# Optimization experiments

Hardware: AMD Instinct MI355X
Metric: run time of the kernel (lower is better)

The kernel has to match this reference:

```python
import jax, jax.numpy as jnp
import numpy as np

B, N, EM = 16, 1024, 768
D_K, D_V, H = 768, 768, 12

def setup_inputs() -> dict:
    key = jax.random.key(0)
    ks = jax.random.split(key, 4)
    s = 0.02
    x = jax.random.normal(ks[0], (B, N, EM), dtype=jnp.float32)
    W_qk = jax.random.normal(ks[1], (EM, 2 * D_K), dtype=jnp.float32) * s
    b_qk = jnp.zeros((2 * D_K,), dtype=jnp.float32)
    W_v = jax.random.normal(ks[2], (EM, D_V), dtype=jnp.float32) * s
    b_v = jnp.zeros((D_V,), dtype=jnp.float32)
    W_proj = jax.random.normal(ks[3], (D_V, EM), dtype=jnp.float32) * s
    b_proj = jnp.zeros((EM,), dtype=jnp.float32)
    return {"x": x, "W_qk": W_qk, "b_qk": b_qk, "W_v": W_v, "b_v": b_v,
            "W_proj": W_proj, "b_proj": b_proj}

def reference(x, W_qk, b_qk, W_v, b_v, W_proj, b_proj):
    b, n, _ = x.shape
    d = D_K // H  # per-head dim
    # qk Linear -> [B,N,2*d_K]; rearrange 'b n (h d qk) -> qk b h n d'
    # i.e. last dim splits as (h, d, 2) with qk fastest-varying.
    qk = (x @ W_qk + b_qk).reshape(b, n, H, d, 2)
    Q = jnp.transpose(qk[..., 0], (0, 2, 1, 3))  # [B,H,N,d]
    K = jnp.transpose(qk[..., 1], (0, 2, 1, 3))  # [B,H,N,d]
    V = (x @ W_v + b_v).reshape(b, n, H, D_V // H).transpose(0, 2, 1, 3)  # [B,H,N,dv]
    scores = jnp.einsum('bhqd,bhkd->bhqk', Q, K) / jnp.sqrt(jnp.float32(d))
    att = jax.nn.softmax(scores, axis=-1)  # dropout p=0 -> identity
    out = jnp.einsum('bhqk,bhkv->bhqv', att, V)  # [B,H,N,dv]
    out = out.transpose(0, 2, 1, 3).reshape(b, n, D_V)
    return out @ W_proj + b_proj
```

## Files before the change

kernel.cpp:

```cpp
#include <hip/hip_runtime.h>
#include <hip/hip_bf16.h>
#include <stdint.h>

typedef unsigned short u16;
typedef __bf16 bf16_t;
typedef bf16_t bf16x8 __attribute__((ext_vector_type(8)));
typedef short s16x4 __attribute__((ext_vector_type(4)));
typedef float f32x4 __attribute__((ext_vector_type(4)));

__device__ __forceinline__ u16 f2bf(float f) {
    union { float f; uint32_t i; } v; v.f = f;
    uint32_t i = v.i;
    uint32_t r = (i + 0x7FFFu + ((i >> 16) & 1u)) >> 16;
    return (u16)r;
}

__device__ __forceinline__ void gload_lds16(const u16* g, u16* l) {
    auto gp = (const __attribute__((address_space(1))) void*)g;
    auto lp = (__attribute__((address_space(3))) void*)(uintptr_t)l;
    __builtin_amdgcn_global_load_lds(gp, lp, 16, 0, 0);
}

__global__ void convert_f32_bf16_kernel(const float* __restrict__ src,
                                        u16* __restrict__ dst, int n4) {
    int i = blockIdx.x * blockDim.x + threadIdx.x;
    if (i < n4) {
        float4 v = ((const float4*)src)[i];
        ushort4 o;
        o.x = f2bf(v.x); o.y = f2bf(v.y); o.z = f2bf(v.z); o.w = f2bf(v.w);
        ((ushort4*)dst)[i] = o;
    }
}

__global__ void transpose_qk_kernel(const float* __restrict__ W, const float* __restrict__ b,
                                    u16* __restrict__ Wt, float* __restrict__ bp) {
    int k = blockIdx.x;
    const float* row = W + (size_t)k * 1536;
    for (int c = threadIdx.x; c < 1536; c += 256) {
        int qk = c & 1;
        int r  = qk * 768 + (c >> 7) * 64 + ((c >> 1) & 63);
        float s = qk ? 1.0f : 0.125f;
        Wt[(size_t)r * 768 + k] = f2bf(s * row[c]);
    }
    if (k == 0) {
        for (int c = threadIdx.x; c < 1536; c += 256) {
            int qk = c & 1;
            int r  = qk * 768 + (c >> 7) * 64 + ((c >> 1) & 63);
            bp[r] = (qk ? 1.0f : 0.125f) * b[c];
        }
    }
}

__global__ void transpose_sq2_kernel(const float* __restrict__ Wv, u16* __restrict__ Wvt,
                                     const float* __restrict__ Wp, u16* __restrict__ Wpt) {
    int id = blockIdx.x;
    const float* W = (id < 768) ? Wv : Wp;
    u16* Wt        = (id < 768) ? Wvt : Wpt;
    int k = (id < 768) ? id : (id - 768);
    const float* row = W + (size_t)k * 768;
    for (int n = threadIdx.x; n < 768; n += 256)
        Wt[(size_t)n * 768 + k] = f2bf(row[n]);
}

__global__ __launch_bounds__(256)
void gemm_qkv_kernel(const u16* __restrict__ A,
                     const u16* __restrict__ Wqkt, const u16* __restrict__ Wvt,
                     const float* __restrict__ bqkp, const float* __restrict__ bv,
                     u16* __restrict__ Qp, u16* __restrict__ Kp, u16* __restrict__ Vp) {
    __shared__ __attribute__((aligned(16))) u16 As[128 * 64];
    __shared__ __attribute__((aligned(16))) u16 Bs[128 * 64];
    const int K = 768;

    const int tid  = threadIdx.x;
    const int lane = tid & 63;
    const int wave = tid >> 6;
    const int l16  = lane & 15;
    const int quad = lane >> 4;
    const int cpx  = 2304 >> 3;
    const int swz  = ((int)blockIdx.x & 7) * cpx + ((int)blockIdx.x >> 3);
    const int mt   = swz / 18;
    const int nt   = swz % 18;
    const bool vmode = nt >= 12;
    const int m0 = mt * 128;
    const int n0 = (vmode ? nt - 12 : nt) * 128;
    const u16* Bt = vmode ? Wvt : Wqkt;
    const float* bias = vmode ? bv : bqkp;
    const int wm = (wave & 1) * 64;
    const int wn = (wave >> 1) * 64;

    f32x4 acc[4][4];
#pragma unroll
    for (int i = 0; i < 4; i++)
#pragma unroll
        for (int j = 0; j < 4; j++) acc[i][j] = (f32x4){0.f, 0.f, 0.f, 0.f};

    const int rs   = lane >> 3;
    const int gseg = (lane & 7) ^ rs;
    const u16* Ag[4]; const u16* Bg[4];
#pragma unroll
    for (int c = 0; c < 4; c++) {
        Ag[c] = A  + (size_t)(m0 + c * 32 + wave * 8 + rs) * K + gseg * 8;
        Bg[c] = Bt + (size_t)(n0 + c * 32 + wave * 8 + rs) * K + gseg * 8;
    }
    u16* AsW = As + wave * 512;
    u16* BsW = Bs + wave * 512;
    const int sw7 = l16 & 7;

    for (int k0 = 0; k0 < K; k0 += 64) {
#pragma unroll
        for (int c = 0; c < 4; c++) {
            gload_lds16(Ag[c] + k0, AsW + c * 2048);
            gload_lds16(Bg[c] + k0, BsW + c * 2048);
        }
        __syncthreads();

        bf16x8 af[4][2], bfr[4][2];
#pragma unroll
        for (int i = 0; i < 4; i++) {
#pragma unroll
            for (int hh = 0; hh < 2; hh++) {
                af[i][hh]  = *(const bf16x8*)&As[(wm + i * 16 + l16) * 64 +
                                                 (((hh * 4 + quad) ^ sw7) * 8)];
                bfr[i][hh] = *(const bf16x8*)&Bs[(wn + i * 16 + l16) * 64 +
                                                 (((hh * 4 + quad) ^ sw7) * 8)];
            }
        }
        if (vmode) {
#pragma unroll
            for (int i = 0; i < 4; i++)
#pragma unroll
                for (int j = 0; j < 4; j++)
#pragma unroll
                    for (int hh = 0; hh < 2; hh++)
                        acc[i][j] = __builtin_amdgcn_mfma_f32_16x16x32_bf16(af[i][hh], bfr[j][hh], acc[i][j], 0, 0, 0);
        } else {
#pragma unroll
            for (int i = 0; i < 4; i++)
#pragma unroll
                for (int j = 0; j < 4; j++)
#pragma unroll
                    for (int hh = 0; hh < 2; hh++)
                        acc[i][j] = __builtin_amdgcn_mfma_f32_16x16x32_bf16(bfr[j][hh], af[i][hh], acc[i][j], 0, 0, 0);
        }
        __syncthreads();
    }

    if (vmode) {
#pragma unroll
        for (int j = 0; j < 4; j++) {
            int cnb = n0 + wn + j * 16;
            int h   = cnb >> 6;
            int dv  = (cnb & 63) + l16;
            float bvv = bias[cnb + l16];
#pragma unroll
            for (int i = 0; i < 4; i++) {
                int cm = m0 + wm + i * 16 + quad * 4;
                int bb = cm >> 10, n = cm & 1023;
                ushort4 o;
                o.x = f2bf(acc[i][j][0] + bvv);
                o.y = f2bf(acc[i][j][1] + bvv);
                o.z = f2bf(acc[i][j][2] + bvv);
                o.w = f2bf(acc[i][j][3] + bvv);
                *(ushort4*)&Vp[((size_t)((bb * 12 + h) * 64 + dv)) * 1024 + n] = o;
            }
        }
    } else {
#pragma unroll
        for (int j = 0; j < 4; j++) {
            int f0 = n0 + wn + j * 16 + quad * 4;
            float4 bv4 = *(const float4*)&bias[f0];
            int qk = f0 >= 768;
            int hd = f0 - qk * 768;
            int h  = hd >> 6;
            int d0 = hd & 63;
            u16* dst = qk ? Kp : Qp;
#pragma unroll
            for (int i = 0; i < 4; i++) {
                int t = m0 + wm + i * 16 + l16;
                int bb = t >> 10, n = t & 1023;
                ushort4 o;
                o.x = f2bf(acc[i][j][0] + bv4.x);
                o.y = f2bf(acc[i][j][1] + bv4.y);
                o.z = f2bf(acc[i][j][2] + bv4.z);
                o.w = f2bf(acc[i][j][3] + bv4.w);
                *(ushort4*)&dst[((size_t)((bb * 12 + h) * 1024 + n)) * 64 + d0] = o;
            }
        }
    }
}

__global__ __launch_bounds__(256)
void gemm_out_kernel(const u16* __restrict__ A, const u16* __restrict__ Bt,
                     const float* __restrict__ bias, float* __restrict__ Cout,
                     int M, int N, int K) {
    __shared__ __attribute__((aligned(16))) u16 As[128 * 64];
    __shared__ __attribute__((aligned(16))) u16 Bs[128 * 64];

    const int tid  = threadIdx.x;
    const int lane = tid & 63;
    const int wave = tid >> 6;
    const int l16  = lane & 15;
    const int quad = lane >> 4;
    const int nxt = N >> 7;
    const int cpx = (int)gridDim.x >> 3;
    const int swz = ((int)blockIdx.x & 7) * cpx + ((int)blockIdx.x >> 3);
    const int m0 = (swz / nxt) * 128;
    const int n0 = (swz % nxt) * 128;
    const int wm = (wave & 1) * 64;
    const int wn = (wave >> 1) * 64;

    f32x4 acc[4][4];
#pragma unroll
    for (int i = 0; i < 4; i++)
#pragma unroll
        for (int j = 0; j < 4; j++) acc[i][j] = (f32x4){0.f, 0.f, 0.f, 0.f};

    const int rs   = lane >> 3;
    const int gseg = (lane & 7) ^ rs;
    const u16* Ag[4]; const u16* Bg[4];
#pragma unroll
    for (int c = 0; c < 4; c++) {
        Ag[c] = A  + (size_t)(m0 + c * 32 + wave * 8 + rs) * K + gseg * 8;
        Bg[c] = Bt + (size_t)(n0 + c * 32 + wave * 8 + rs) * K + gseg * 8;
    }
    u16* AsW = As + wave * 512;
    u16* BsW = Bs + wave * 512;
    const int sw7 = l16 & 7;

    for (int k0 = 0; k0 < K; k0 += 64) {
#pragma unroll
        for (int c = 0; c < 4; c++) {
            gload_lds16(Ag[c] + k0, AsW + c * 2048);
            gload_lds16(Bg[c] + k0, BsW + c * 2048);
        }
        __syncthreads();

        bf16x8 af[4][2], bfr[4][2];
#pragma unroll
        for (int i = 0; i < 4; i++) {
#pragma unroll
            for (int hh = 0; hh < 2; hh++) {
                af[i][hh]  = *(const bf16x8*)&As[(wm + i * 16 + l16) * 64 +
                                                 (((hh * 4 + quad) ^ sw7) * 8)];
                bfr[i][hh] = *(const bf16x8*)&Bs[(wn + i * 16 + l16) * 64 +
                                                 (((hh * 4 + quad) ^ sw7) * 8)];
            }
        }
#pragma unroll
        for (int i = 0; i < 4; i++)
#pragma unroll
            for (int j = 0; j < 4; j++)
#pragma unroll
                for (int hh = 0; hh < 2; hh++)
                    acc[i][j] = __builtin_amdgcn_mfma_f32_16x16x32_bf16(bfr[j][hh], af[i][hh], acc[i][j], 0, 0, 0);
        __syncthreads();
    }

#pragma unroll
    for (int j = 0; j < 4; j++) {
        int f0 = n0 + wn + j * 16 + quad * 4;
        float4 bv = *(const float4*)&bias[f0];
#pragma unroll
        for (int i = 0; i < 4; i++) {
            int t = m0 + wm + i * 16 + l16;
            float4 o;
            o.x = acc[i][j][0] + bv.x;
            o.y = acc[i][j][1] + bv.y;
            o.z = acc[i][j][2] + bv.z;
            o.w = acc[i][j][3] + bv.w;
            *(float4*)&Cout[(size_t)t * N + f0] = o;
        }
    }
}

__global__ __launch_bounds__(512)
void attention_mfma_kernel(const u16* __restrict__ Qp, const u16* __restrict__ Kp,
                           const u16* __restrict__ Vp, u16* __restrict__ attout) {
    __shared__ __attribute__((aligned(16))) u16 Ks[2][64 * 64];
    __shared__ __attribute__((aligned(16))) u16 Vs[2][64 * 64];

    const int tid  = threadIdx.x;
    const int wave = tid >> 6;
    const int lane = tid & 63;
    const int l16  = lane & 15;
    const int quad = lane >> 4;
    const int flat = blockIdx.x;
    const int swz  = (flat & 7) * 96 + (flat >> 3);
    const int bh   = swz >> 2;
    const int b    = bh / 12, h = bh % 12;
    const int q0   = (swz & 3) * 256 + wave * 32;

    const u16* Qhead = Qp + (size_t)bh * 1024 * 64;
    const u16* Khead = Kp + (size_t)bh * 1024 * 64;
    const u16* Vhead = Vp + (size_t)bh * 64 * 1024;

    bf16x8 qf[2][2];
#pragma unroll
    for (int qb = 0; qb < 2; qb++) {
        const u16* qrow = Qhead + (size_t)(q0 + qb * 16 + l16) * 64;
        qf[qb][0] = *(const bf16x8*)(qrow + quad * 8);
        qf[qb][1] = *(const bf16x8*)(qrow + 32 + quad * 8);
    }

    f32x4 oacc[2][4];
#pragma unroll
    for (int qb = 0; qb < 2; qb++)
#pragma unroll
        for (int db = 0; db < 4; db++) oacc[qb][db] = (f32x4){0.f, 0.f, 0.f, 0.f};
    float l_part[2] = {0.f, 0.f};

    const int srow = tid >> 3;
    const int gseg = (tid & 7) ^ (srow & 7);
    const u16* Kg = Khead + (size_t)srow * 64 + gseg * 8;
    const u16* Vg = Vhead + (size_t)srow * 1024 + gseg * 8;
    const int sw7 = l16 & 7;

    gload_lds16(Kg, &Ks[0][wave * 512]);
    gload_lds16(Vg, &Vs[0][wave * 512]);

    int cur = 0;
    for (int t = 0; t < 16; ++t) {
        __syncthreads();
        if (t < 15) {
            gload_lds16(Kg + (t + 1) * 4096, &Ks[cur ^ 1][wave * 512]);
            gload_lds16(Vg + (t + 1) * 64,   &Vs[cur ^ 1][wave * 512]);
        }
        const u16* Ksc = Ks[cur];
        const u16* Vsc = Vs[cur];

        union { uint32_t u[4]; bf16x8 v; } pf8[2][2];
        {
            bf16x8 kf[4][2];
#pragma unroll
            for (int jb = 0; jb < 4; jb++) {
#pragma unroll
                for (int hf = 0; hf < 2; hf++)
                    kf[jb][hf] = *(const bf16x8*)&Ksc[(jb * 16 + l16) * 64 +
                                                      (((hf * 4 + quad) ^ sw7) * 8)];
            }
#pragma unroll
            for (int qb = 0; qb < 2; qb++) {
#pragma unroll
                for (int jb = 0; jb < 4; jb++) {
                    f32x4 st = (f32x4){0.f, 0.f, 0.f, 0.f};
                    __builtin_amdgcn_s_setprio(1);
                    st = __builtin_amdgcn_mfma_f32_16x16x32_bf16(kf[jb][0], qf[qb][0], st, 0, 0, 0);
                    st = __builtin_amdgcn_mfma_f32_16x16x32_bf16(kf[jb][1], qf[qb][1], st, 0, 0, 0);
                    __builtin_amdgcn_s_setprio(0);
                    float e0 = __expf(st[0]), e1 = __expf(st[1]);
                    float e2 = __expf(st[2]), e3 = __expf(st[3]);
                    l_part[qb] += (e0 + e1) + (e2 + e3);
                    union { __hip_bfloat162 h2; uint32_t u; } c0, c1;
                    c0.h2 = __float22bfloat162_rn(make_float2(e0, e1));
                    c1.h2 = __float22bfloat162_rn(make_float2(e2, e3));
                    pf8[qb][jb >> 1].u[(jb & 1) * 2 + 0] = c0.u;
                    pf8[qb][jb >> 1].u[(jb & 1) * 2 + 1] = c1.u;
                }
            }
        }

        __builtin_amdgcn_s_setprio(1);
#pragma unroll
        for (int db = 0; db < 4; db++) {
#pragma unroll
            for (int jp = 0; jp < 2; jp++) {
                union { s16x4 hh[2]; bf16x8 v; } vb8;
                int glo = 4 * jp + (quad >> 1);
                int ghi = glo + 2;
                vb8.hh[0] = *(const s16x4*)&Vsc[(db * 16 + l16) * 64 +
                                                ((glo ^ sw7) * 8) + (quad & 1) * 4];
                vb8.hh[1] = *(const s16x4*)&Vsc[(db * 16 + l16) * 64 +
                                                ((ghi ^ sw7) * 8) + (quad & 1) * 4];
#pragma unroll
                for (int qb = 0; qb < 2; qb++)
                    oacc[qb][db] = __builtin_amdgcn_mfma_f32_16x16x32_bf16(
                        pf8[qb][jp].v, vb8.v, oacc[qb][db], 0, 0, 0);
            }
        }
        __builtin_amdgcn_s_setprio(0);
        cur ^= 1;
    }

#pragma unroll
    for (int qb = 0; qb < 2; qb++) {
        float l = l_part[qb];
        l += __shfl_xor(l, 16);
        l += __shfl_xor(l, 32);
        float linv[4];
#pragma unroll
        for (int r = 0; r < 4; r++)
            linv[r] = 1.0f / __shfl(l, quad * 4 + r);
        u16* orow = attout + (size_t)(b * 1024 + q0 + qb * 16 + quad * 4) * 768 + h * 64 + l16;
#pragma unroll
        for (int db = 0; db < 4; db++)
#pragma unroll
            for (int r = 0; r < 4; r++)
                orow[(size_t)r * 768 + db * 16] = f2bf(oacc[qb][db][r] * linv[r]);
    }
}

extern "C" void kernel_launch(void* const* d_in, const int* in_sizes, int n_in,
                              void* d_out, int out_size, void* d_ws, size_t ws_size,
                              hipStream_t stream) {
    const float* x      = (const float*)d_in[0];
    const float* W_qk   = (const float*)d_in[1];
    const float* b_qk   = (const float*)d_in[2];
    const float* W_v    = (const float*)d_in[3];
    const float* b_v    = (const float*)d_in[4];
    const float* W_proj = (const float*)d_in[5];
    const float* b_proj = (const float*)d_in[6];
    float* out = (float*)d_out;

    char* ws = (char*)d_ws;
    size_t off = 0;
    auto alloc = [&](size_t bytes) { void* p = ws + off; off += (bytes + 255) & ~255ull; return p; };
    u16*   xb     = (u16*)alloc((size_t)16384 * 768 * 2);
    u16*   Wqkt   = (u16*)alloc((size_t)1536 * 768 * 2);
    float* bqkp   = (float*)alloc(1536 * 4);
    u16*   Wvt    = (u16*)alloc((size_t)768 * 768 * 2);
    u16*   Wprojt = (u16*)alloc((size_t)768 * 768 * 2);
    u16*   Qp     = (u16*)alloc((size_t)16384 * 768 * 2);
    u16*   Kp     = (u16*)alloc((size_t)16384 * 768 * 2);
    u16*   Vp     = (u16*)alloc((size_t)16384 * 768 * 2);
    u16*   attout = (u16*)alloc((size_t)16384 * 768 * 2);

    convert_f32_bf16_kernel<<<12288, 256, 0, stream>>>(x, xb, 3145728);
    transpose_qk_kernel<<<768, 256, 0, stream>>>(W_qk, b_qk, Wqkt, bqkp);
    transpose_sq2_kernel<<<1536, 256, 0, stream>>>(W_v, Wvt, W_proj, Wprojt);

    gemm_qkv_kernel<<<2304, 256, 0, stream>>>(xb, Wqkt, Wvt, bqkp, b_v, Qp, Kp, Vp);
    attention_mfma_kernel<<<768, 512, 0, stream>>>(Qp, Kp, Vp, attout);
    gemm_out_kernel<<<768, 256, 0, stream>>>(attout, Wprojt, b_proj, out, 16384, 768, 768);
}
```

Baseline: 338.3 us.

## Double-buffer LDS tiles in QKV and output GEMMs to overlap loads with MFMA

Both projection GEMMs now use two LDS buffers per operand. The next k-tile is issued with global_load_lds while the current tile is consumed by MFMAs, and one of the two barriers per iteration is removed. Wave priority is raised around the MFMA block. This aims to hide global load latency, at the cost of doubling shared memory per block, which may lower occupancy.

Result: faster. 326.9 us (-3.4%).

```diff
diff --git a/kernel.cpp b/kernel.cpp
--- a/kernel.cpp
+++ b/kernel.cpp
@@ -67,8 +67,8 @@
                      const u16* __restrict__ Wqkt, const u16* __restrict__ Wvt,
                      const float* __restrict__ bqkp, const float* __restrict__ bv,
                      u16* __restrict__ Qp, u16* __restrict__ Kp, u16* __restrict__ Vp) {
-    __shared__ __attribute__((aligned(16))) u16 As[128 * 64];
-    __shared__ __attribute__((aligned(16))) u16 Bs[128 * 64];
+    __shared__ __attribute__((aligned(16))) u16 As[2][128 * 64];
+    __shared__ __attribute__((aligned(16))) u16 Bs[2][128 * 64];
     const int K = 768;
 
     const int tid  = threadIdx.x;
@@ -102,29 +102,39 @@
         Ag[c] = A  + (size_t)(m0 + c * 32 + wave * 8 + rs) * K + gseg * 8;
         Bg[c] = Bt + (size_t)(n0 + c * 32 + wave * 8 + rs) * K + gseg * 8;
     }
-    u16* AsW = As + wave * 512;
-    u16* BsW = Bs + wave * 512;
     const int sw7 = l16 & 7;
 
-    for (int k0 = 0; k0 < K; k0 += 64) {
-#pragma unroll
-        for (int c = 0; c < 4; c++) {
-            gload_lds16(Ag[c] + k0, AsW + c * 2048);
-            gload_lds16(Bg[c] + k0, BsW + c * 2048);
-        }
+#pragma unroll
+    for (int c = 0; c < 4; c++) {
+        gload_lds16(Ag[c], &As[0][wave * 512 + c * 2048]);
+        gload_lds16(Bg[c], &Bs[0][wave * 512 + c * 2048]);
+    }
+
+    int cur = 0;
+    for (int t = 0; t < 12; ++t) {
         __syncthreads();
+        if (t < 11) {
+#pragma unroll
+            for (int c = 0; c < 4; c++) {
+                gload_lds16(Ag[c] + (t + 1) * 64, &As[cur ^ 1][wave * 512 + c * 2048]);
+                gload_lds16(Bg[c] + (t + 1) * 64, &Bs[cur ^ 1][wave * 512 + c * 2048]);
+            }
+        }
+        const u16* Asc = As[cur];
+        const u16* Bsc = Bs[cur];
 
         bf16x8 af[4][2], bfr[4][2];
 #pragma unroll
         for (int i = 0; i < 4; i++) {
 #pragma unroll
             for (int hh = 0; hh < 2; hh++) {
-                af[i][hh]  = *(const bf16x8*)&As[(wm + i * 16 + l16) * 64 +
-                                                 (((hh * 4 + quad) ^ sw7) * 8)];
-                bfr[i][hh] = *(const bf16x8*)&Bs[(wn + i * 16 + l16) * 64 +
-                                                 (((hh * 4 + quad) ^ sw7) * 8)];
-            }
-        }
+                af[i][hh]  = *(const bf16x8*)&Asc[(wm + i * 16 + l16) * 64 +
+                                                  (((hh * 4 + quad) ^ sw7) * 8)];
+                bfr[i][hh] = *(const bf16x8*)&Bsc[(wn + i * 16 + l16) * 64 +
+                                                  (((hh * 4 + quad) ^ sw7) * 8)];
+            }
+        }
+        __builtin_amdgcn_s_setprio(1);
         if (vmode) {
 #pragma unroll
             for (int i = 0; i < 4; i++)
@@ -142,7 +152,8 @@
                     for (int hh = 0; hh < 2; hh++)
                         acc[i][j] = __builtin_amdgcn_mfma_f32_16x16x32_bf16(bfr[j][hh], af[i][hh], acc[i][j], 0, 0, 0);
         }
-        __syncthreads();
+        __builtin_amdgcn_s_setprio(0);
+        cur ^= 1;
     }
 
     if (vmode) {
@@ -193,8 +204,8 @@
 void gemm_out_kernel(const u16* __restrict__ A, const u16* __restrict__ Bt,
                      const float* __restrict__ bias, float* __restrict__ Cout,
                      int M, int N, int K) {
-    __shared__ __attribute__((aligned(16))) u16 As[128 * 64];
-    __shared__ __attribute__((aligned(16))) u16 Bs[128 * 64];
+    __shared__ __attribute__((aligned(16))) u16 As[2][128 * 64];
+    __shared__ __attribute__((aligned(16))) u16 Bs[2][128 * 64];
 
     const int tid  = threadIdx.x;
     const int lane = tid & 63;
@@ -223,29 +234,40 @@
         Ag[c] = A  + (size_t)(m0 + c * 32 + wave * 8 + rs) * K + gseg * 8;
         Bg[c] = Bt + (size_t)(n0 + c * 32 + wave * 8 + rs) * K + gseg * 8;
     }
-    u16* AsW = As + wave * 512;
-    u16* BsW = Bs + wave * 512;
     const int sw7 = l16 & 7;
-
-    for (int k0 = 0; k0 < K; k0 += 64) {
-#pragma unroll
-        for (int c = 0; c < 4; c++) {
-            gload_lds16(Ag[c] + k0, AsW + c * 2048);
-            gload_lds16(Bg[c] + k0, BsW + c * 2048);
-        }
+    const int nk = K >> 6;
+
+#pragma unroll
+    for (int c = 0; c < 4; c++) {
+        gload_lds16(Ag[c], &As[0][wave * 512 + c * 2048]);
+        gload_lds16(Bg[c], &Bs[0][wave * 512 + c * 2048]);
+    }
+
+    int cur = 0;
+    for (int t = 0; t < nk; ++t) {
         __syncthreads();
+        if (t < nk - 1) {
+#pragma unroll
+            for (int c = 0; c < 4; c++) {
+                gload_lds16(Ag[c] + (t + 1) * 64, &As[cur ^ 1][wave * 512 + c * 2048]);
+                gload_lds16(Bg[c] + (t + 1) * 64, &Bs[cur ^ 1][wave * 512 + c * 2048]);
+            }
+        }
+        const u16* Asc = As[cur];
+        const u16* Bsc = Bs[cur];
 
         bf16x8 af[4][2], bfr[4][2];
 #pragma unroll
         for (int i = 0; i < 4; i++) {
 #pragma unroll
             for (int hh = 0; hh < 2; hh++) {
-                af[i][hh]  = *(const bf16x8*)&As[(wm + i * 16 + l16) * 64 +
-                                                 (((hh * 4 + quad) ^ sw7) * 8)];
-                bfr[i][hh] = *(const bf16x8*)&Bs[(wn + i * 16 + l16) * 64 +
-                                                 (((hh * 4 + quad) ^ sw7) * 8)];
-            }
-        }
+                af[i][hh]  = *(const bf16x8*)&Asc[(wm + i * 16 + l16) * 64 +
+                                                  (((hh * 4 + quad) ^ sw7) * 8)];
+                bfr[i][hh] = *(const bf16x8*)&Bsc[(wn + i * 16 + l16) * 64 +
+                                                  (((hh * 4 + quad) ^ sw7) * 8)];
+            }
+        }
+        __builtin_amdgcn_s_setprio(1);
 #pragma unroll
         for (int i = 0; i < 4; i++)
 #pragma unroll
@@ -253,7 +275,8 @@
 #pragma unroll
                 for (int hh = 0; hh < 2; hh++)
                     acc[i][j] = __builtin_amdgcn_mfma_f32_16x16x32_bf16(bfr[j][hh], af[i][hh], acc[i][j], 0, 0, 0);
-        __syncthreads();
+        __builtin_amdgcn_s_setprio(0);
+        cur ^= 1;
     }
 
 #pragma unroll
```
